# Kernel optimization log

Hardware: AMD Instinct MI355X
Metric: run time of the kernel (lower is better)

The kernel has to match this reference:

```python
import jax, jax.numpy as jnp
import numpy as np

N, DIN, DOUT, E, K = 65536, 256, 256, 8, 2

def setup_inputs() -> dict:
    key = jax.random.key(0)
    k1, k2, k3, k4 = jax.random.split(key, 4)
    x = jax.random.normal(k1, (N, DIN), dtype=jnp.float32)
    Wr = jax.random.normal(k2, (DIN, E), dtype=jnp.float32) * (DIN ** -0.5)   # router Linear (no bias)
    We = jax.random.normal(k3, (E, DIN, DOUT), dtype=jnp.float32) * (DIN ** -0.5)  # expert Linear weights
    be = jax.random.normal(k4, (E, DOUT), dtype=jnp.float32) * 0.01               # expert Linear biases
    return {"x": x, "Wr": Wr, "We": We, "be": be}

def reference(x, Wr, We, be):
    # router: softmax over experts (eval mode -> no noise)
    probs = jax.nn.softmax(x @ Wr, axis=1)                    # [N, E]
    w, sel = jax.lax.top_k(probs, K)                          # [N, K]
    w = w / jnp.sum(w, axis=1, keepdims=True)                 # renormalize top-k weights
    # dense combine weights: scatter top-k weights back to [N, E]
    combine = jnp.zeros_like(probs).at[jnp.arange(x.shape[0])[:, None], sel].add(w)
    # all-expert outputs, then weighted combine (same math as gather/matmul/index_add loop)
    y_all = jnp.einsum('ni,eio->neo', x, We) + be[None, :, :]  # [N, E, DOUT]
    out = jnp.einsum('neo,ne->no', y_all, combine)             # [N, DOUT]
    return out
```

## Files before the change

kernel.cpp:

```cpp
#include <hip/hip_runtime.h>

#define N_TOK 65536
#define DIN   256
#define DOUT  256
#define NEXP  8
#define NPAIR 28

typedef __bf16 bf16x8 __attribute__((ext_vector_type(8)));
typedef __bf16 bf16x4 __attribute__((ext_vector_type(4)));
typedef float  f32x4  __attribute__((ext_vector_type(4)));

__device__ __forceinline__ void cp16_g2l(const void* g, void* l) {
  auto gp = (const __attribute__((address_space(1))) unsigned int*)(unsigned long long)g;
  auto lp = (__attribute__((address_space(3))) unsigned int*)(unsigned long long)l;
  __builtin_amdgcn_global_load_lds(gp, lp, 16, 0, 0);
}

__global__ __launch_bounds__(256) void prep_kernel(const float* __restrict__ We,
                                                   __bf16* __restrict__ Wt,
                                                   int* __restrict__ cnt) {
  __shared__ float T[64 * 65];
  int bid = blockIdx.x;
  if (bid == 0 && threadIdx.x < NPAIR) cnt[threadIdx.x] = 0;
  int e = bid >> 4;
  int tk = (bid >> 2) & 3, tn = bid & 3;
  int k0 = tk * 64, n0 = tn * 64;
  int tid = threadIdx.x;
  int cr = tid >> 6;
  int cc = tid & 63;
#pragma unroll
  for (int i = 0; i < 16; i++) {
    int k = i * 4 + cr;
    T[cc * 65 + k] = We[(size_t)(e * 256 + k0 + k) * 256 + n0 + cc];
  }
  __syncthreads();
#pragma unroll
  for (int i = 0; i < 16; i++) {
    int n = i * 4 + cr;
    Wt[(size_t)(e * 256 + n0 + n) * 256 + k0 + cc] = (__bf16)T[n * 65 + cc];
  }
}

__global__ __launch_bounds__(256) void router_kernel(const float* __restrict__ x,
                                                     const float* __restrict__ Wr,
                                                     __bf16* __restrict__ xb,
                                                     int* __restrict__ cnt,
                                                     unsigned short* __restrict__ pidx,
                                                     float* __restrict__ pw) {
  __shared__ float X[64 * 64];
  __shared__ float P[64 * 36];
  __shared__ int lcnt[NPAIR];
  __shared__ int gbase[NPAIR];
  int tid = threadIdx.x;
  if (tid < NPAIR) lcnt[tid] = 0;

  const int w = __builtin_amdgcn_readfirstlane(tid >> 6);
  const int t = tid & 63;
  int tokBase = blockIdx.x * 64;

  const int srow = tid >> 4;
  const int so16 = tid & 15;
  const int spo  = so16 ^ (srow & 7);

  float acc[NEXP];
#pragma unroll
  for (int e = 0; e < NEXP; e++) acc[e] = 0.f;

  float4 v[4];
#pragma unroll
  for (int i = 0; i < 4; i++)
    v[i] = *(const float4*)&x[(size_t)(tokBase + srow + 16 * i) * DIN + so16 * 4];

  for (int c = 0; c < 4; c++) {
#pragma unroll
    for (int i = 0; i < 4; i++) {
      int r = srow + 16 * i;
      *(float4*)&X[r * 64 + spo * 4] = v[i];
      bf16x4 bv;
      bv[0] = (__bf16)v[i].x; bv[1] = (__bf16)v[i].y;
      bv[2] = (__bf16)v[i].z; bv[3] = (__bf16)v[i].w;
      *(bf16x4*)&xb[(size_t)(tokBase + r) * DIN + c * 64 + so16 * 4] = bv;
    }
    __syncthreads();
    if (c < 3) {
#pragma unroll
      for (int i = 0; i < 4; i++)
        v[i] = *(const float4*)&x[(size_t)(tokBase + srow + 16 * i) * DIN + (c + 1) * 64 + so16 * 4];
    }
#pragma unroll
    for (int i4 = 0; i4 < 4; i4++) {
      int po = (w * 4 + i4) ^ (t & 7);
      float4 xv = *(const float4*)&X[t * 64 + po * 4];
      const float* w0 = &Wr[(c * 64 + w * 16 + i4 * 4) * NEXP];
#pragma unroll
      for (int e = 0; e < NEXP; e++)
        acc[e] += xv.x * w0[e] + xv.y * w0[NEXP + e] + xv.z * w0[2 * NEXP + e] + xv.w * w0[3 * NEXP + e];
    }
    __syncthreads();
  }

  f32x4 lo, hi;
#pragma unroll
  for (int e = 0; e < 4; e++) { lo[e] = acc[e]; hi[e] = acc[4 + e]; }
  *(f32x4*)&P[t * 36 + w * 8]     = lo;
  *(f32x4*)&P[t * 36 + w * 8 + 4] = hi;
  __syncthreads();
  if (tid >= 64) return;

  int token = tokBase + tid;

  f32x4 pa0 = *(const f32x4*)&P[tid * 36 + 0];
  f32x4 pa1 = *(const f32x4*)&P[tid * 36 + 8];
  f32x4 pa2 = *(const f32x4*)&P[tid * 36 + 16];
  f32x4 pa3 = *(const f32x4*)&P[tid * 36 + 24];
  f32x4 pb0 = *(const f32x4*)&P[tid * 36 + 4];
  f32x4 pb1 = *(const f32x4*)&P[tid * 36 + 12];
  f32x4 pb2 = *(const f32x4*)&P[tid * 36 + 20];
  f32x4 pb3 = *(const f32x4*)&P[tid * 36 + 28];
  f32x4 sA = ((pa0 + pa1) + pa2) + pa3;
  f32x4 sB = ((pb0 + pb1) + pb2) + pb3;
  float lg[NEXP];
#pragma unroll
  for (int e = 0; e < 4; e++) { lg[e] = sA[e]; lg[4 + e] = sB[e]; }

  int best = 0;
#pragma unroll
  for (int e = 1; e < NEXP; e++) if (lg[e] > lg[best]) best = e;
  int sec = (best == 0) ? 1 : 0;
#pragma unroll
  for (int e = 0; e < NEXP; e++)
    if (e != best && e != sec && lg[e] > lg[sec]) sec = e;
  float l3 = -1e30f;
#pragma unroll
  for (int e = 0; e < NEXP; e++)
    if (e != best && e != sec) l3 = fmaxf(l3, lg[e]);

  float diff = lg[sec] - lg[best];
  bool need = (lg[sec] - l3) < 5e-3f;
  if (__any(need)) {
    if (need) {
      const float4* xr = (const float4*)(x + (size_t)token * DIN);
      double d[NEXP];
#pragma unroll
      for (int e = 0; e < NEXP; e++) d[e] = 0.0;
      for (int i4 = 0; i4 < DIN / 4; i4++) {
        float4 vv = xr[i4];
        const float* w0 = &Wr[(i4 * 4) * NEXP];
#pragma unroll
        for (int e = 0; e < NEXP; e++)
          d[e] += (double)vv.x * w0[e] + (double)vv.y * w0[NEXP + e] +
                  (double)vv.z * w0[2 * NEXP + e] + (double)vv.w * w0[3 * NEXP + e];
      }
      best = 0;
#pragma unroll
      for (int e = 1; e < NEXP; e++) if (d[e] > d[best]) best = e;
      sec = (best == 0) ? 1 : 0;
#pragma unroll
      for (int e = 0; e < NEXP; e++)
        if (e != best && e != sec && d[e] > d[sec]) sec = e;
      diff = (float)(d[sec] - d[best]);
    }
  }

  float wb = 1.f / (1.f + expf(diff));
  int a, b2; float wa;
  if (best < sec) { a = best; b2 = sec; wa = wb; }
  else            { a = sec;  b2 = best; wa = 1.f - wb; }
  int p = a * (15 - a) / 2 + (b2 - a - 1);

  int lpos = atomicAdd(&lcnt[p], 1);
  if (tid < NPAIR) gbase[tid] = atomicAdd(&cnt[tid], lcnt[tid]);
  int pos = gbase[p] + lpos;
  pidx[p * N_TOK + pos] = (unsigned short)token;
  pw[p * N_TOK + pos] = wa;
}

__global__ __launch_bounds__(256) void moe_gemm_kernel(const __bf16* __restrict__ xb,
                                                       const __bf16* __restrict__ Wt,
                                                       const float* __restrict__ be,
                                                       const int* __restrict__ cnt,
                                                       const unsigned short* __restrict__ pidx,
                                                       const float* __restrict__ pw,
                                                       float* __restrict__ out) {
  __shared__ __bf16 As[128 * 64];
  __shared__ unsigned short tokL[128];
  __shared__ float wL[128];
  __shared__ int meta[4];

  int tid = threadIdx.x;
  int tile = blockIdx.x >> 2;
  int nh = blockIdx.x & 3;

  if (tid == 0) {
    int s = 0, pp = -1, lt = 0, c = 0;
    for (int q = 0; q < NPAIR; q++) {
      int cq = cnt[q];
      int tq = (cq + 127) >> 7;
      if (tile < s + tq) { pp = q; lt = tile - s; c = cq; break; }
      s += tq;
    }
    meta[0] = pp; meta[1] = lt; meta[2] = c;
  }
  __syncthreads();
  int p = meta[0];
  if (p < 0) return;
  int lt = meta[1], cnt_p = meta[2];

  int a = 0, rem = p;
  while (rem >= 7 - a) { rem -= 7 - a; a++; }
  int b2 = a + 1 + rem;
  int r0 = lt * 128;

  if (tid < 128) {
    int gr = r0 + tid;
    tokL[tid] = (gr < cnt_p) ? pidx[p * N_TOK + gr] : (unsigned short)0;
    wL[tid]   = (gr < cnt_p) ? pw[p * N_TOK + gr] : 0.f;
  }
  __syncthreads();

  const int lane = tid & 63, wid = tid >> 6;
  const int wm = wid & 1, wn = wid >> 1;
  const int c16 = lane & 15, quad = lane >> 4;

  const int r_base = tid >> 3;
  const int s8 = (tid & 7) ^ (r_base & 7);
  size_t grow[4];
#pragma unroll
  for (int i = 0; i < 4; i++)
    grow[i] = (size_t)tokL[r_base + 32 * i] * DIN + s8 * 8;

  const __bf16* WtA = Wt + ((size_t)a * DOUT + nh * 64) * DIN;
  const __bf16* WtB = Wt + ((size_t)b2 * DOUT + nh * 64) * DIN;

  f32x4 accA[4][2], accB[4][2];
#pragma unroll
  for (int mi = 0; mi < 4; mi++)
#pragma unroll
    for (int ni = 0; ni < 2; ni++)
#pragma unroll
      for (int r = 0; r < 4; r++) { accA[mi][ni][r] = 0.f; accB[mi][ni][r] = 0.f; }

  for (int kc = 0; kc < 4; kc++) {
#pragma unroll
    for (int i = 0; i < 4; i++) {
      int slot = tid + 256 * i;
      cp16_g2l(xb + grow[i] + kc * 64, &As[slot * 8]);
    }
    __builtin_amdgcn_s_waitcnt(0x0F70);
    __syncthreads();
#pragma unroll
    for (int ks = 0; ks < 2; ks++) {
      bf16x8 af[4], ba[2], bb[2];
#pragma unroll
      for (int mi = 0; mi < 4; mi++) {
        int row = wm * 64 + mi * 16 + c16;
        int oct = ks * 4 + quad;
        af[mi] = *(const bf16x8*)&As[(row * 8 + (oct ^ (row & 7))) * 8];
      }
#pragma unroll
      for (int ni = 0; ni < 2; ni++) {
        int col = wn * 32 + ni * 16 + c16;
        int koff = kc * 64 + ks * 32 + quad * 8;
        ba[ni] = *(const bf16x8*)&WtA[(size_t)col * DIN + koff];
        bb[ni] = *(const bf16x8*)&WtB[(size_t)col * DIN + koff];
      }
#pragma unroll
      for (int mi = 0; mi < 4; mi++)
#pragma unroll
        for (int ni = 0; ni < 2; ni++) {
          accA[mi][ni] = __builtin_amdgcn_mfma_f32_16x16x32_bf16(af[mi], ba[ni], accA[mi][ni], 0, 0, 0);
          accB[mi][ni] = __builtin_amdgcn_mfma_f32_16x16x32_bf16(af[mi], bb[ni], accB[mi][ni], 0, 0, 0);
        }
    }
    __syncthreads();
  }

#pragma unroll
  for (int ni = 0; ni < 2; ni++) {
    int gcol = nh * 64 + wn * 32 + ni * 16 + c16;
    float bea = be[a * DOUT + gcol];
    float beb = be[b2 * DOUT + gcol];
#pragma unroll
    for (int mi = 0; mi < 4; mi++) {
#pragma unroll
      for (int r = 0; r < 4; r++) {
        int row = wm * 64 + mi * 16 + quad * 4 + r;
        if (r0 + row < cnt_p) {
          float w = wL[row];
          out[(size_t)tokL[row] * DOUT + gcol] =
              w * (accA[mi][ni][r] + bea) + (1.f - w) * (accB[mi][ni][r] + beb);
        }
      }
    }
  }
}

extern "C" void kernel_launch(void* const* d_in, const int* in_sizes, int n_in,
                              void* d_out, int out_size, void* d_ws, size_t ws_size,
                              hipStream_t stream) {
  const float* x  = (const float*)d_in[0];
  const float* Wr = (const float*)d_in[1];
  const float* We = (const float*)d_in[2];
  const float* be = (const float*)d_in[3];
  float* out = (float*)d_out;

  char* w = (char*)d_ws;
  __bf16* Wt = (__bf16*)w;
  __bf16* xb = (__bf16*)(w + (1u << 20));
  int* cnt = (int*)(w + (33u << 20));
  unsigned short* pidx = (unsigned short*)(w + (33u << 20) + 512);
  float* pw = (float*)(w + (33u << 20) + 512 + (size_t)NPAIR * N_TOK * 2);

  prep_kernel<<<128, 256, 0, stream>>>(We, Wt, cnt);
  router_kernel<<<N_TOK / 64, 256, 0, stream>>>(x, Wr, xb, cnt, pidx, pw);
  moe_gemm_kernel<<<540 * 4, 256, 0, stream>>>(xb, Wt, be, cnt, pidx, pw, out);
}
```

Baseline: 212.7 us.

## Use 512-thread full-width blocks with triple-buffered async A staging

Each block now covers all 256 output columns for a 128-token pair tile with 8 waves, instead of four blocks each covering 64 columns. The gathered x rows are therefore loaded once rather than four times. The four K-chunks are staged into a triple-buffered LDS ring with async global-to-LDS copies and explicit waitcnt/barrier so loads overlap MFMA work. The cost is higher register pressure (32 accumulators per wave), more LDS (48KB), and fewer blocks available to fill the GPU.

```diff
diff --git a/kernel.cpp b/kernel.cpp
--- a/kernel.cpp
+++ b/kernel.cpp
@@ -15,6 +15,10 @@
   auto lp = (__attribute__((address_space(3))) unsigned int*)(unsigned long long)l;
   __builtin_amdgcn_global_load_lds(gp, lp, 16, 0, 0);
 }
+
+#define BARRIER() do { asm volatile("" ::: "memory"); \
+                       __builtin_amdgcn_s_barrier();  \
+                       asm volatile("" ::: "memory"); } while (0)
 
 __global__ __launch_bounds__(256) void prep_kernel(const float* __restrict__ We,
                                                    __bf16* __restrict__ Wt,
@@ -175,21 +179,20 @@
   pw[p * N_TOK + pos] = wa;
 }
 
-__global__ __launch_bounds__(256) void moe_gemm_kernel(const __bf16* __restrict__ xb,
-                                                       const __bf16* __restrict__ Wt,
-                                                       const float* __restrict__ be,
-                                                       const int* __restrict__ cnt,
-                                                       const unsigned short* __restrict__ pidx,
-                                                       const float* __restrict__ pw,
-                                                       float* __restrict__ out) {
-  __shared__ __bf16 As[128 * 64];
+__global__ __launch_bounds__(512, 2) void moe_gemm_kernel(const __bf16* __restrict__ xb,
+                                                          const __bf16* __restrict__ Wt,
+                                                          const float* __restrict__ be,
+                                                          const int* __restrict__ cnt,
+                                                          const unsigned short* __restrict__ pidx,
+                                                          const float* __restrict__ pw,
+                                                          float* __restrict__ out) {
+  __shared__ __bf16 As[3][128 * 64];
   __shared__ unsigned short tokL[128];
   __shared__ float wL[128];
   __shared__ int meta[4];
 
   int tid = threadIdx.x;
-  int tile = blockIdx.x >> 2;
-  int nh = blockIdx.x & 3;
+  int tile = blockIdx.x;
 
   if (tid == 0) {
     int s = 0, pp = -1, lt = 0, c = 0;
@@ -222,62 +225,75 @@
   const int wm = wid & 1, wn = wid >> 1;
   const int c16 = lane & 15, quad = lane >> 4;
 
-  const int r_base = tid >> 3;
-  const int s8 = (tid & 7) ^ (r_base & 7);
-  size_t grow[4];
-#pragma unroll
-  for (int i = 0; i < 4; i++)
-    grow[i] = (size_t)tokL[r_base + 32 * i] * DIN + s8 * 8;
-
-  const __bf16* WtA = Wt + ((size_t)a * DOUT + nh * 64) * DIN;
-  const __bf16* WtB = Wt + ((size_t)b2 * DOUT + nh * 64) * DIN;
-
-  f32x4 accA[4][2], accB[4][2];
+  const int rs0 = tid >> 3;
+  const int s8 = (tid & 7) ^ (rs0 & 7);
+  const size_t g0 = (size_t)tokL[rs0] * DIN + s8 * 8;
+  const size_t g1 = (size_t)tokL[rs0 + 64] * DIN + s8 * 8;
+
+  const __bf16* WtA = Wt + (size_t)a  * (DOUT * DIN);
+  const __bf16* WtB = Wt + (size_t)b2 * (DOUT * DIN);
+
+  f32x4 accA[4][4], accB[4][4];
 #pragma unroll
   for (int mi = 0; mi < 4; mi++)
 #pragma unroll
-    for (int ni = 0; ni < 2; ni++)
+    for (int ni = 0; ni < 4; ni++)
 #pragma unroll
       for (int r = 0; r < 4; r++) { accA[mi][ni][r] = 0.f; accB[mi][ni][r] = 0.f; }
 
-  for (int kc = 0; kc < 4; kc++) {
-#pragma unroll
-    for (int i = 0; i < 4; i++) {
-      int slot = tid + 256 * i;
-      cp16_g2l(xb + grow[i] + kc * 64, &As[slot * 8]);
-    }
-    __builtin_amdgcn_s_waitcnt(0x0F70);
-    __syncthreads();
+  auto STAGE = [&](int B, int KC) {
+    cp16_g2l(xb + g0 + KC * 64, &As[B][tid * 8]);
+    cp16_g2l(xb + g1 + KC * 64, &As[B][(tid + 512) * 8]);
+  };
+
+  auto COMPUTE = [&](int B, int KC) {
 #pragma unroll
     for (int ks = 0; ks < 2; ks++) {
-      bf16x8 af[4], ba[2], bb[2];
+      bf16x8 af[4];
+      int oct = ks * 4 + quad;
 #pragma unroll
       for (int mi = 0; mi < 4; mi++) {
         int row = wm * 64 + mi * 16 + c16;
-        int oct = ks * 4 + quad;
-        af[mi] = *(const bf16x8*)&As[(row * 8 + (oct ^ (row & 7))) * 8];
+        af[mi] = *(const bf16x8*)&As[B][(row * 8 + (oct ^ (row & 7))) * 8];
       }
 #pragma unroll
-      for (int ni = 0; ni < 2; ni++) {
-        int col = wn * 32 + ni * 16 + c16;
-        int koff = kc * 64 + ks * 32 + quad * 8;
-        ba[ni] = *(const bf16x8*)&WtA[(size_t)col * DIN + koff];
-        bb[ni] = *(const bf16x8*)&WtB[(size_t)col * DIN + koff];
+      for (int ni = 0; ni < 4; ni++) {
+        int col = wn * 64 + ni * 16 + c16;
+        int koff = KC * 64 + ks * 32 + quad * 8;
+        bf16x8 ba = *(const bf16x8*)&WtA[(size_t)col * DIN + koff];
+        bf16x8 bb = *(const bf16x8*)&WtB[(size_t)col * DIN + koff];
+#pragma unroll
+        for (int mi = 0; mi < 4; mi++) {
+          accA[mi][ni] = __builtin_amdgcn_mfma_f32_16x16x32_bf16(af[mi], ba, accA[mi][ni], 0, 0, 0);
+          accB[mi][ni] = __builtin_amdgcn_mfma_f32_16x16x32_bf16(af[mi], bb, accB[mi][ni], 0, 0, 0);
+        }
       }
-#pragma unroll
-      for (int mi = 0; mi < 4; mi++)
-#pragma unroll
-        for (int ni = 0; ni < 2; ni++) {
-          accA[mi][ni] = __builtin_amdgcn_mfma_f32_16x16x32_bf16(af[mi], ba[ni], accA[mi][ni], 0, 0, 0);
-          accB[mi][ni] = __builtin_amdgcn_mfma_f32_16x16x32_bf16(af[mi], bb[ni], accB[mi][ni], 0, 0, 0);
-        }
-    }
-    __syncthreads();
-  }
-
-#pragma unroll
-  for (int ni = 0; ni < 2; ni++) {
-    int gcol = nh * 64 + wn * 32 + ni * 16 + c16;
+    }
+  };
+
+  STAGE(0, 0);
+  STAGE(1, 1);
+  asm volatile("s_waitcnt vmcnt(2)" ::: "memory");
+  BARRIER();
+  STAGE(2, 2);
+  COMPUTE(0, 0);
+  asm volatile("s_waitcnt lgkmcnt(0)" ::: "memory");
+  asm volatile("s_waitcnt vmcnt(2)" ::: "memory");
+  BARRIER();
+  STAGE(0, 3);
+  COMPUTE(1, 1);
+  asm volatile("s_waitcnt lgkmcnt(0)" ::: "memory");
+  asm volatile("s_waitcnt vmcnt(2)" ::: "memory");
+  BARRIER();
+  COMPUTE(2, 2);
+  asm volatile("s_waitcnt lgkmcnt(0)" ::: "memory");
+  asm volatile("s_waitcnt vmcnt(0)" ::: "memory");
+  BARRIER();
+  COMPUTE(0, 3);
+
+#pragma unroll
+  for (int ni = 0; ni < 4; ni++) {
+    int gcol = wn * 64 + ni * 16 + c16;
     float bea = be[a * DOUT + gcol];
     float beb = be[b2 * DOUT + gcol];
 #pragma unroll
@@ -313,5 +329,5 @@
 
   prep_kernel<<<128, 256, 0, stream>>>(We, Wt, cnt);
   router_kernel<<<N_TOK / 64, 256, 0, stream>>>(x, Wr, xb, cnt, pidx, pw);
-  moe_gemm_kernel<<<540 * 4, 256, 0, stream>>>(xb, Wt, be, cnt, pidx, pw, out);
-}
+  moe_gemm_kernel<<<540, 512, 0, stream>>>(xb, Wt, be, cnt, pidx, pw, out);
+}
```

After: 228.5 us. +7.5%, slower.
